# Kernel optimization log

Hardware: AMD Instinct MI355X
Metric: run time of the kernel (lower is better)

## Reference

```python
import jax, jax.numpy as jnp
import numpy as np
import math

D_MODEL = 128      # embedding_dim
D_STATE = 64
D_CONV = 4
NHEADS = 4         # d_inner / headdim (Mamba2 default headdim=64)
HEADDIM = 64
D_INNER = 256      # expand * d_model
CONV_DIM = 384     # d_inner + 2*ngroups*d_state (ngroups=1)
D_IN_PROJ = 644    # 2*d_inner + 2*ngroups*d_state + nheads
NLAYERS = 2
INPUT_DIM = 768
EPS = 1e-5


def setup_inputs() -> dict:
    key = jax.random.key(0)
    ks = jax.random.split(key, 20)
    rn = lambda k, s, sd=0.02: jax.random.normal(k, s, jnp.float32) * sd
    return {
        "x": jax.random.normal(ks[0], (16, 1024, INPUT_DIM), jnp.float32),
        "fc1_W": rn(ks[1], (INPUT_DIM, D_MODEL)),
        "fc1_b": jnp.zeros((D_MODEL,), jnp.float32),
        "ln_w": jnp.ones((NLAYERS, D_MODEL), jnp.float32),
        "ln_b": jnp.zeros((NLAYERS, D_MODEL), jnp.float32),
        "in_W": rn(ks[2], (NLAYERS, D_MODEL, D_IN_PROJ)),
        "conv_w": rn(ks[3], (NLAYERS, D_CONV, CONV_DIM), 0.1),
        "conv_b": jnp.zeros((NLAYERS, CONV_DIM), jnp.float32),
        "dt_bias": rn(ks[4], (NLAYERS, NHEADS), 0.5),
        "A_log": jnp.log(jax.random.uniform(ks[5], (NLAYERS, NHEADS), jnp.float32, 1.0, 16.0)),
        "Dp": jnp.ones((NLAYERS, NHEADS), jnp.float32),
        "rms_w": jnp.ones((NLAYERS, D_INNER), jnp.float32),
        "out_W": rn(ks[6], (NLAYERS, D_INNER, D_MODEL)),
        "fc2_W1": rn(ks[7], (D_MODEL, D_MODEL)),
        "fc2_b1": jnp.zeros((D_MODEL,), jnp.float32),
        "fc2_W2": rn(ks[8], (D_MODEL, 6)),
        "fc2_b2": jnp.zeros((6,), jnp.float32),
    }


def _pos_embedding(L):
    pos = jnp.arange(L, dtype=jnp.float32)[:, None]                       # (L,1)
    div = jnp.exp(jnp.arange(0, D_MODEL, 2, dtype=jnp.float32) * (-math.log(10000.0) / D_MODEL))
    pe = jnp.zeros((L, D_MODEL), jnp.float32)
    pe = pe.at[:, 0::2].set(jnp.sin(pos * div))
    pe = pe.at[:, 1::2].set(jnp.cos(pos * div))
    return pe[None]                                                        # (1,L,D)


def _layernorm(x, w, b):
    mu = jnp.mean(x, -1, keepdims=True)
    var = jnp.mean(jnp.square(x - mu), -1, keepdims=True)
    return (x - mu) * jax.lax.rsqrt(var + EPS) * w + b


def _mamba2(u, in_W, conv_w, conv_b, dt_bias, A_log, Dp, rms_w, out_W):
    b, l, _ = u.shape
    zxbcdt = u @ in_W                                                      # (b,l,644)
    z = zxbcdt[..., :D_INNER]
    xBC = zxbcdt[..., D_INNER:D_INNER + CONV_DIM]
    dt = jax.nn.softplus(zxbcdt[..., D_INNER + CONV_DIM:] + dt_bias)       # (b,l,h)
    # causal depthwise conv1d (width 4) + SiLU
    xp = jnp.pad(xBC, ((0, 0), (D_CONV - 1, 0), (0, 0)))
    xc = conv_b
    for k in range(D_CONV):
        xc = xc + conv_w[k] * xp[:, k:k + l, :]
    xc = jax.nn.silu(xc)                                                   # (b,l,384)
    xh = xc[..., :D_INNER].reshape(b, l, NHEADS, HEADDIM)                  # (b,l,h,p)
    B = xc[..., D_INNER:D_INNER + D_STATE]                                 # (b,l,n)
    C = xc[..., D_INNER + D_STATE:]                                        # (b,l,n)
    A = -jnp.exp(A_log)                                                    # (h,)
    dA = jnp.exp(dt * A)                                                   # (b,l,h)
    dtx = dt[..., None] * xh                                               # (b,l,h,p)

    def step(h, inp):
        dA_t, dtx_t, B_t, C_t = inp                                        # (b,h),(b,h,p),(b,n),(b,n)
        h = dA_t[..., None, None] * h + dtx_t[..., None] * B_t[:, None, None, :]
        y = jnp.einsum('bhpn,bn->bhp', h, C_t)
        return h, y

    h0 = jnp.zeros((b, NHEADS, HEADDIM, D_STATE), u.dtype)
    _, ys = jax.lax.scan(step, h0, (dA.transpose(1, 0, 2), dtx.transpose(1, 0, 2, 3),
                                    B.transpose(1, 0, 2), C.transpose(1, 0, 2)))
    y = ys.transpose(1, 0, 2, 3) + Dp[None, None, :, None] * xh            # (b,l,h,p)
    y = y.reshape(b, l, D_INNER)
    # gated RMSNorm: rmsnorm(y * silu(z)) * weight
    y = y * jax.nn.silu(z)
    y = y * jax.lax.rsqrt(jnp.mean(jnp.square(y), -1, keepdims=True) + EPS) * rms_w
    return y @ out_W


def reference(x, fc1_W, fc1_b, ln_w, ln_b, in_W, conv_w, conv_b, dt_bias,
              A_log, Dp, rms_w, out_W, fc2_W1, fc2_b1, fc2_W2, fc2_b2):
    h = x @ fc1_W + fc1_b                                                  # (b,l,128)
    h = h + _pos_embedding(h.shape[1])
    for i in range(NLAYERS):
        res = h
        hn = _layernorm(h, ln_w[i], ln_b[i])
        h = _mamba2(hn, in_W[i], conv_w[i], conv_b[i], dt_bias[i],
                    A_log[i], Dp[i], rms_w[i], out_W[i]) + res
        # dropout: identity in eval mode
    h = jax.nn.leaky_relu(h @ fc2_W1 + fc2_b1, negative_slope=0.1)
    return h @ fc2_W2 + fc2_b2                                             # (b,l,6)
```

## Files before the change

### kernel.cpp

```cpp
#include <hip/hip_runtime.h>
#include <hip/hip_bf16.h>

#define BATCH 16
#define SEQ 1024
#define NROWS (BATCH*SEQ)
#define IN_DIM 768
#define DM 128
#define DIP 644
#define DI 256
#define CDIM 384
#define DST 64
#define NH 4
#define HD 64
#define CHUNK 64
#define NCHUNK (SEQ/CHUNK)

#define WB_FC1   0
#define WB_IN    98304
#define WB_OUT   263168
#define WB_FC2   328704
#define WB_TOTAL 345088

typedef __attribute__((ext_vector_type(8))) short short8;
typedef __attribute__((ext_vector_type(4))) float float4v;

__device__ __forceinline__ short f2b(float f) {
    unsigned u = __builtin_bit_cast(unsigned, f);
    u += 0x7fffu + ((u >> 16) & 1u);
    return (short)(u >> 16);
}
__device__ __forceinline__ float s2f(short s) {
    unsigned u = ((unsigned)(unsigned short)s) << 16;
    return __builtin_bit_cast(float, u);
}
__device__ __forceinline__ short8 pack8f(float4 a, float4 b) {
    short8 r;
    r[0] = f2b(a.x); r[1] = f2b(a.y); r[2] = f2b(a.z); r[3] = f2b(a.w);
    r[4] = f2b(b.x); r[5] = f2b(b.y); r[6] = f2b(b.z); r[7] = f2b(b.w);
    return r;
}
__device__ __forceinline__ float silu(float a) { return a / (1.f + expf(-a)); }

__global__ void prep_weights(const float* __restrict__ fc1_W, const float* __restrict__ in_W,
                             const float* __restrict__ out_W, const float* __restrict__ fc2_W1,
                             short* __restrict__ wb) {
    int idx = blockIdx.x * 256 + threadIdx.x;
    if (idx < 98304) {
        int n = idx / 768, k = idx % 768;
        wb[WB_FC1 + idx] = f2b(fc1_W[k * 128 + n]);
        return;
    }
    idx -= 98304;
    if (idx < 2 * 82432) {
        int l = idx / 82432, r = idx % 82432;
        int n = r / 128, k = r % 128;
        wb[WB_IN + idx] = f2b(in_W[(size_t)l * 82432 + k * 644 + n]);
        return;
    }
    idx -= 164864;
    if (idx < 2 * 32768) {
        int l = idx / 32768, r = idx % 32768;
        int n = r / 256, k = r % 256;
        wb[WB_OUT + idx] = f2b(out_W[(size_t)l * 32768 + k * 128 + n]);
        return;
    }
    idx -= 65536;
    if (idx < 16384) {
        int n = idx / 128, k = idx % 128;
        wb[WB_FC2 + idx] = f2b(fc2_W1[k * 128 + n]);
    }
}

#define GEMM_PROLOGUE() \
    int tid = threadIdx.x; \
    int lane = tid & 63; \
    int m = lane & 15; \
    int kq = (lane >> 4) * 8; \
    int w = tid >> 6; \
    int mrow = (w & 3) * 16; \
    int ngrp = w >> 2; \
    int a_off = (mrow + m) * 72 + kq; \
    int b_off = (ngrp * 64 + m) * 72 + kq; \
    int ar = tid >> 3; \
    int ak = (tid & 7) * 8; \
    (void)ar; (void)ak; \
    float4v acc[4]; \
    acc[0] = (float4v)0.f; acc[1] = (float4v)0.f; acc[2] = (float4v)0.f; acc[3] = (float4v)0.f;

#define GEMM_COMPUTE_TILE() \
    { \
        short8 a0 = *reinterpret_cast<const short8*>(&As[a_off]); \
        short8 a1 = *reinterpret_cast<const short8*>(&As[a_off + 32]); \
        _Pragma("unroll") \
        for (int nt = 0; nt < 4; nt++) { \
            short8 b0 = *reinterpret_cast<const short8*>(&Bt[b_off + nt * 16 * 72]); \
            short8 b1 = *reinterpret_cast<const short8*>(&Bt[b_off + nt * 16 * 72 + 32]); \
            acc[nt] = __builtin_amdgcn_mfma_f32_16x16x32_bf16(a0, b0, acc[nt], 0, 0, 0); \
            acc[nt] = __builtin_amdgcn_mfma_f32_16x16x32_bf16(a1, b1, acc[nt], 0, 0, 0); \
        } \
    }

#define GEMM_STAGE_B(wtptr, LDB, k0) \
    _Pragma("unroll") \
    for (int i = 0; i < 2; i++) { \
        int idx = tid + i * 512; \
        int n = idx >> 3, kk = (idx & 7) * 8; \
        *reinterpret_cast<short8*>(&Bt[n * 72 + kk]) = \
            *reinterpret_cast<const short8*>(&wtptr[n * (LDB) + (k0) + kk]); \
    }

__global__ __launch_bounds__(512) void fc1_mfma(const float* __restrict__ x,
                                                const short* __restrict__ wt,
                                                const float* __restrict__ bias,
                                                const float* __restrict__ lnw0,
                                                const float* __restrict__ lnb0,
                                                float* __restrict__ h,
                                                short* __restrict__ hnb) {
    __shared__ __align__(16) char smem[64 * 133 * 4];
    short* As = (short*)smem;
    short* Bt = (short*)(smem + 64 * 72 * 2);
    float* hs = (float*)smem;
    GEMM_PROLOGUE();
    int row0 = blockIdx.x * 64;
    for (int kt = 0; kt < 12; kt++) {
        int k0 = kt * 64;
        if (kt) __syncthreads();
        {
            const float* src = x + (size_t)(row0 + ar) * IN_DIM + k0 + ak;
            float4 v0 = *(const float4*)src;
            float4 v1 = *(const float4*)(src + 4);
            *reinterpret_cast<short8*>(&As[ar * 72 + ak]) = pack8f(v0, v1);
        }
        GEMM_STAGE_B(wt, 768, k0);
        __syncthreads();
        GEMM_COMPUTE_TILE();
    }
    __syncthreads();
    #pragma unroll
    for (int nt = 0; nt < 4; nt++) {
        int col = ngrp * 64 + nt * 16 + m;
        float bv = bias[col];
        float div = expf(-(float)(col & ~1) * 0.071955784f);
        #pragma unroll
        for (int r = 0; r < 4; r++) {
            int rr = mrow + (lane >> 4) * 4 + r;
            int t = (row0 + rr) & (SEQ - 1);
            float arg = (float)t * div;
            float pe = (col & 1) ? cosf(arg) : sinf(arg);
            hs[rr * 133 + col] = acc[nt][r] + bv + pe;
        }
    }
    __syncthreads();
    {
        int r = tid >> 3, j = tid & 7;
        int row = row0 + r;
        float vals[16]; float s1 = 0.f, s2 = 0.f;
        #pragma unroll
        for (int i = 0; i < 16; i++) {
            float v = hs[r * 133 + j * 16 + i];
            vals[i] = v; s1 += v; s2 += v * v;
        }
        #pragma unroll
        for (int o = 1; o < 8; o <<= 1) { s1 += __shfl_xor(s1, o); s2 += __shfl_xor(s2, o); }
        float mu = s1 * (1.f / 128.f);
        float rs = rsqrtf(s2 * (1.f / 128.f) - mu * mu + 1e-5f);
        float* hdst = h + (size_t)row * DM + j * 16;
        #pragma unroll
        for (int i = 0; i < 4; i++)
            *(float4*)(hdst + i * 4) = make_float4(vals[i*4], vals[i*4+1], vals[i*4+2], vals[i*4+3]);
        const float* lw = lnw0 + j * 16;
        const float* lb = lnb0 + j * 16;
        short8 a0, a1;
        #pragma unroll
        for (int i = 0; i < 8; i++) {
            a0[i] = f2b((vals[i] - mu) * rs * lw[i] + lb[i]);
            a1[i] = f2b((vals[8 + i] - mu) * rs * lw[8 + i] + lb[8 + i]);
        }
        short* hndst = hnb + (size_t)row * DM + j * 16;
        *reinterpret_cast<short8*>(hndst) = a0;
        *reinterpret_cast<short8*>(hndst + 8) = a1;
    }
}

__global__ __launch_bounds__(512) void inproj_mfma(const short* __restrict__ hnb,
                                                   const short* __restrict__ wb,
                                                   short* __restrict__ zb,
                                                   short* __restrict__ xbc,
                                                   float* __restrict__ dtb,
                                                   const float* __restrict__ dt_bias, int layer) {
    __shared__ short As[64 * 72];
    __shared__ short Bt[128 * 72];
    GEMM_PROLOGUE();
    int row0 = blockIdx.x * 64;
    int ncol0 = blockIdx.y * 128;
    const short* wt = wb + WB_IN + (size_t)layer * 82432;
    for (int kt = 0; kt < 2; kt++) {
        int k0 = kt * 64;
        if (kt) __syncthreads();
        *reinterpret_cast<short8*>(&As[ar * 72 + ak]) =
            *reinterpret_cast<const short8*>(&hnb[(size_t)(row0 + ar) * DM + k0 + ak]);
        #pragma unroll
        for (int i = 0; i < 2; i++) {
            int idx = tid + i * 512;
            int n = idx >> 3, kk = (idx & 7) * 8;
            int col = ncol0 + n;
            short8 bv = (short8)0;
            if (col < DIP) bv = *reinterpret_cast<const short8*>(&wt[col * 128 + k0 + kk]);
            *reinterpret_cast<short8*>(&Bt[n * 72 + kk]) = bv;
        }
        __syncthreads();
        GEMM_COMPUTE_TILE();
    }
    #pragma unroll
    for (int nt = 0; nt < 4; nt++) {
        int col = ncol0 + ngrp * 64 + nt * 16 + m;
        if (col < DI) {
            #pragma unroll
            for (int r = 0; r < 4; r++) {
                int row = row0 + mrow + (lane >> 4) * 4 + r;
                zb[(size_t)row * DI + col] = f2b(acc[nt][r]);
            }
        } else if (col < DI + CDIM) {
            #pragma unroll
            for (int r = 0; r < 4; r++) {
                int row = row0 + mrow + (lane >> 4) * 4 + r;
                xbc[(size_t)row * CDIM + (col - DI)] = f2b(acc[nt][r]);
            }
        } else if (col < DIP) {
            int hh = col - DI - CDIM;
            float db = dt_bias[layer * NH + hh];
            #pragma unroll
            for (int r = 0; r < 4; r++) {
                int row = row0 + mrow + (lane >> 4) * 4 + r;
                float raw = acc[nt][r] + db;
                float dt = (raw > 20.f) ? raw : log1pf(expf(raw));
                dtb[(size_t)row * NH + hh] = dt;
            }
        }
    }
}

__global__ void conv_kernel(const short* __restrict__ xbc,
                            const float* __restrict__ convw, const float* __restrict__ convb,
                            short* __restrict__ xcb, int layer) {
    int c = threadIdx.x;
    int row0 = blockIdx.x * 4;
    int l0 = row0 & (SEQ - 1);
    const float* cw = convw + (size_t)layer * 4 * CDIM;
    float w0 = cw[c], w1 = cw[CDIM + c], w2 = cw[2 * CDIM + c], w3 = cw[3 * CDIM + c];
    float bb = convb[layer * CDIM + c];
    float v[7];
    #pragma unroll
    for (int i = 0; i < 7; i++) {
        int rr = row0 + i - 3;
        v[i] = (l0 + i - 3 >= 0) ? s2f(xbc[(size_t)rr * CDIM + c]) : 0.f;
    }
    #pragma unroll
    for (int j = 0; j < 4; j++) {
        float acc = bb + w0 * v[j] + w1 * v[j + 1] + w2 * v[j + 2] + w3 * v[j + 3];
        xcb[(size_t)(row0 + j) * CDIM + c] = f2b(silu(acc));
    }
}

__global__ __launch_bounds__(256) void chunk_state_mfma(const short* __restrict__ xcb,
                                                        const float* __restrict__ dtb,
                                                        const float* __restrict__ A_log,
                                                        short* __restrict__ Slocb,
                                                        float* __restrict__ decay, int layer) {
    __shared__ short XTw[64 * 72];
    __shared__ short BT[64 * 72];
    __shared__ float wst[64];
    int bid = blockIdx.x;
    int c  = bid & (NCHUNK - 1);
    int hh = (bid >> 4) & (NH - 1);
    int b  = bid >> 6;
    int tid = threadIdx.x;
    int row0 = b * SEQ + c * CHUNK;
    float A = -expf(A_log[layer * NH + hh]);

    if (tid < CHUNK) {
        float dtv = dtb[(size_t)(row0 + tid) * NH + hh];
        float l = dtv * A;
        #pragma unroll
        for (int o = 1; o < 64; o <<= 1) { float v = __shfl_up(l, o); if (tid >= o) l += v; }
        float Ltot = __shfl(l, 63);
        wst[tid] = expf(Ltot - l) * dtv;
        if (tid == 63) decay[bid] = expf(Ltot);
    }
    __syncthreads();
    {
        int p = tid & 63;
        int tb0 = tid >> 6;
        #pragma unroll
        for (int i = 0; i < 2; i++) {
            int t0 = (tb0 + i * 4) * 8;
            short8 xv, bv;
            #pragma unroll
            for (int j = 0; j < 8; j++) {
                int t = t0 + j;
                const short* xr = xcb + (size_t)(row0 + t) * CDIM;
                xv[j] = f2b(s2f(xr[hh * HD + p]) * wst[t]);
                bv[j] = xr[DI + p];
            }
            *reinterpret_cast<short8*>(&XTw[p * 72 + t0]) = xv;
            *reinterpret_cast<short8*>(&BT[p * 72 + t0]) = bv;
        }
    }
    __syncthreads();

    int lane = tid & 63;
    int m = lane & 15;
    int kq = (lane >> 4) * 8;
    int w = tid >> 6;
    int a_off = (w * 16 + m) * 72 + kq;
    float4v acc[4];
    acc[0] = (float4v)0.f; acc[1] = (float4v)0.f; acc[2] = (float4v)0.f; acc[3] = (float4v)0.f;
    short8 a0 = *reinterpret_cast<const short8*>(&XTw[a_off]);
    short8 a1 = *reinterpret_cast<const short8*>(&XTw[a_off + 32]);
    #pragma unroll
    for (int nt = 0; nt < 4; nt++) {
        int bo = (nt * 16 + m) * 72 + kq;
        short8 b0 = *reinterpret_cast<const short8*>(&BT[bo]);
        short8 b1 = *reinterpret_cast<const short8*>(&BT[bo + 32]);
        acc[nt] = __builtin_amdgcn_mfma_f32_16x16x32_bf16(a0, b0, acc[nt], 0, 0, 0);
        acc[nt] = __builtin_amdgcn_mfma_f32_16x16x32_bf16(a1, b1, acc[nt], 0, 0, 0);
    }
    short* Sp = Slocb + (size_t)bid * (HD * DST);
    int tq = (lane >> 4) * 4;
    #pragma unroll
    for (int nt = 0; nt < 4; nt++) {
        #pragma unroll
        for (int r = 0; r < 4; r++) {
            int p = w * 16 + tq + r;
            int n = nt * 16 + m;
            Sp[p * DST + n] = f2b(acc[nt][r]);
        }
    }
}

__global__ void chunk_scan_kernel(const short* __restrict__ Slocb, const float* __restrict__ decay,
                                  short* __restrict__ hstrb) {
    int bh = blockIdx.x;
    int tid = threadIdx.x;
    float hreg[16];
    #pragma unroll
    for (int k = 0; k < 16; k++) hreg[k] = 0.f;
    for (int c = 0; c < NCHUNK; c++) {
        size_t base = ((size_t)bh * NCHUNK + c) * (HD * DST) + tid * 16;
        float d = decay[bh * NCHUNK + c];
        short8 s0 = *reinterpret_cast<const short8*>(&Slocb[base]);
        short8 s1 = *reinterpret_cast<const short8*>(&Slocb[base + 8]);
        short8 h0, h1;
        #pragma unroll
        for (int k = 0; k < 8; k++) { h0[k] = f2b(hreg[k]); h1[k] = f2b(hreg[8 + k]); }
        *reinterpret_cast<short8*>(&hstrb[base]) = h0;
        *reinterpret_cast<short8*>(&hstrb[base + 8]) = h1;
        #pragma unroll
        for (int k = 0; k < 8; k++) {
            hreg[k]     = d * hreg[k]     + s2f(s0[k]);
            hreg[8 + k] = d * hreg[8 + k] + s2f(s1[k]);
        }
    }
}

__global__ __launch_bounds__(256) void chunk_out_mfma(const short* __restrict__ xcb,
                                                      const float* __restrict__ dtb,
                                                      const float* __restrict__ A_log,
                                                      const float* __restrict__ Dpw,
                                                      const short* __restrict__ hstrb,
                                                      short* __restrict__ ybb, int layer) {
    __shared__ short Cb[64 * 72];
    __shared__ short Bb[64 * 72];
    __shared__ short XT[64 * 72];
    __shared__ short HT[64 * 72];
    __shared__ float Ls[64], dts[64];
    int bid = blockIdx.x;
    int c  = bid & (NCHUNK - 1);
    int hh = (bid >> 4) & (NH - 1);
    int b  = bid >> 6;
    int tid = threadIdx.x;
    int row0 = b * SEQ + c * CHUNK;
    float A = -expf(A_log[layer * NH + hh]);
    float Dph = Dpw[layer * NH + hh];

    if (tid < CHUNK) {
        float dtv = dtb[(size_t)(row0 + tid) * NH + hh];
        float l = dtv * A;
        #pragma unroll
        for (int o = 1; o < 64; o <<= 1) { float v = __shfl_up(l, o); if (tid >= o) l += v; }
        Ls[tid] = l;
        dts[tid] = dtv;
    }
    {
        int p = tid & 63;
        int tb0 = tid >> 6;
        #pragma unroll
        for (int i = 0; i < 2; i++) {
            int t0 = (tb0 + i * 4) * 8;
            short8 xv;
            #pragma unroll
            for (int j = 0; j < 8; j++)
                xv[j] = xcb[(size_t)(row0 + t0 + j) * CDIM + hh * HD + p];
            *reinterpret_cast<short8*>(&XT[p * 72 + t0]) = xv;
        }
    }
    #pragma unroll
    for (int i = 0; i < 2; i++) {
        int idx = tid + i * 256;
        int t = idx >> 3, cb = (idx & 7) * 8;
        const short* xr = xcb + (size_t)(row0 + t) * CDIM;
        *reinterpret_cast<short8*>(&Bb[t * 72 + cb]) =
            *reinterpret_cast<const short8*>(&xr[DI + cb]);
        *reinterpret_cast<short8*>(&Cb[t * 72 + cb]) =
            *reinterpret_cast<const short8*>(&xr[DI + DST + cb]);
    }
    {
        const short* hs = hstrb + (size_t)bid * (HD * DST);
        #pragma unroll
        for (int i = 0; i < 2; i++) {
            int idx = tid + i * 256;
            int pp = idx >> 3, nb = (idx & 7) * 8;
            *reinterpret_cast<short8*>(&HT[pp * 72 + nb]) =
                *reinterpret_cast<const short8*>(&hs[pp * 64 + nb]);
        }
    }
    __syncthreads();

    int lane = tid & 63;
    int m = lane & 15;
    int kq = (lane >> 4) * 8;
    int w = tid >> 6;
    int tq = (lane >> 4) * 4;
    int a_off = (w * 16 + m) * 72 + kq;

    short8 ca0 = *reinterpret_cast<const short8*>(&Cb[a_off]);
    short8 ca1 = *reinterpret_cast<const short8*>(&Cb[a_off + 32]);

    float4v g[4], ir[4];
    #pragma unroll
    for (int i = 0; i < 4; i++) { g[i] = (float4v)0.f; ir[i] = (float4v)0.f; }
    #pragma unroll
    for (int st = 0; st < 4; st++) {
        int bo = (st * 16 + m) * 72 + kq;
        short8 b0 = *reinterpret_cast<const short8*>(&Bb[bo]);
        short8 b1 = *reinterpret_cast<const short8*>(&Bb[bo + 32]);
        g[st] = __builtin_amdgcn_mfma_f32_16x16x32_bf16(ca0, b0, g[st], 0, 0, 0);
        g[st] = __builtin_amdgcn_mfma_f32_16x16x32_bf16(ca1, b1, g[st], 0, 0, 0);
        short8 h0 = *reinterpret_cast<const short8*>(&HT[bo]);
        short8 h1 = *reinterpret_cast<const short8*>(&HT[bo + 32]);
        ir[st] = __builtin_amdgcn_mfma_f32_16x16x32_bf16(ca0, h0, ir[st], 0, 0, 0);
        ir[st] = __builtin_amdgcn_mfma_f32_16x16x32_bf16(ca1, h1, ir[st], 0, 0, 0);
    }
    __syncthreads();
    #pragma unroll
    for (int st = 0; st < 4; st++) {
        #pragma unroll
        for (int r = 0; r < 4; r++) {
            int t = w * 16 + tq + r;
            int s = st * 16 + m;
            float mv = 0.f;
            if (s <= t) mv = g[st][r] * expf(Ls[t] - Ls[s]) * dts[s];
            Bb[t * 72 + s] = f2b(mv);
        }
    }
    __syncthreads();
    float4v yi[4];
    #pragma unroll
    for (int i = 0; i < 4; i++) yi[i] = (float4v)0.f;
    short8 ma0 = *reinterpret_cast<const short8*>(&Bb[a_off]);
    short8 ma1 = *reinterpret_cast<const short8*>(&Bb[a_off + 32]);
    #pragma unroll
    for (int pt = 0; pt < 4; pt++) {
        int bo = (pt * 16 + m) * 72 + kq;
        short8 x0 = *reinterpret_cast<const short8*>(&XT[bo]);
        short8 x1 = *reinterpret_cast<const short8*>(&XT[bo + 32]);
        yi[pt] = __builtin_amdgcn_mfma_f32_16x16x32_bf16(ma0, x0, yi[pt], 0, 0, 0);
        yi[pt] = __builtin_amdgcn_mfma_f32_16x16x32_bf16(ma1, x1, yi[pt], 0, 0, 0);
    }
    #pragma unroll
    for (int r = 0; r < 4; r++) {
        int t = w * 16 + tq + r;
        float et = expf(Ls[t]);
        short* yr = ybb + (size_t)(row0 + t) * DI + hh * HD;
        #pragma unroll
        for (int pt = 0; pt < 4; pt++) {
            int p = pt * 16 + m;
            float xv = s2f(XT[p * 72 + t]);
            yr[p] = f2b(yi[pt][r] + et * ir[pt][r] + Dph * xv);
        }
    }
}

__global__ __launch_bounds__(512) void outproj_gate_mfma(const short* __restrict__ ybb,
                                                         const short* __restrict__ zb,
                                                         const float* __restrict__ rmsw,
                                                         const short* __restrict__ wb,
                                                         const float* __restrict__ lnw2,
                                                         const float* __restrict__ lnb2,
                                                         float* __restrict__ h,
                                                         short* __restrict__ hnb,
                                                         int layer, int write_hn) {
    __shared__ __align__(16) char smem[64 * 133 * 4];
    short* As = (short*)smem;
    short* Bt = (short*)(smem + 64 * 72 * 2);
    float* hs = (float*)smem;
    __shared__ float rs_s[64];
    GEMM_PROLOGUE();
    int row0 = blockIdx.x * 64;
    const short* wt = wb + WB_OUT + (size_t)layer * 32768;
    {
        int r = tid >> 3, j = tid & 7;
        const short8* yr = (const short8*)(ybb + (size_t)(row0 + r) * DI + j * 32);
        const short8* zr = (const short8*)(zb + (size_t)(row0 + r) * DI + j * 32);
        float s2 = 0.f;
        #pragma unroll
        for (int i = 0; i < 4; i++) {
            short8 yv = yr[i];
            short8 zv = zr[i];
            #pragma unroll
            for (int q = 0; q < 8; q++) {
                float v = s2f(yv[q]) * silu(s2f(zv[q]));
                s2 += v * v;
            }
        }
        #pragma unroll
        for (int o = 1; o < 8; o <<= 1) s2 += __shfl_xor(s2, o);
        if (j == 0) rs_s[r] = rsqrtf(s2 * (1.f / 256.f) + 1e-5f);
    }
    __syncthreads();
    for (int kt = 0; kt < 4; kt++) {
        int k0 = kt * 64;
        if (kt) __syncthreads();
        {
            int k = k0 + ak;
            short8 yv = *(const short8*)(ybb + (size_t)(row0 + ar) * DI + k);
            short8 zv = *(const short8*)(zb + (size_t)(row0 + ar) * DI + k);
            float4 w0 = *(const float4*)(rmsw + layer * DI + k);
            float4 w1 = *(const float4*)(rmsw + layer * DI + k + 4);
            float rs = rs_s[ar];
            short8 av;
            av[0] = f2b(s2f(yv[0]) * silu(s2f(zv[0])) * rs * w0.x);
            av[1] = f2b(s2f(yv[1]) * silu(s2f(zv[1])) * rs * w0.y);
            av[2] = f2b(s2f(yv[2]) * silu(s2f(zv[2])) * rs * w0.z);
            av[3] = f2b(s2f(yv[3]) * silu(s2f(zv[3])) * rs * w0.w);
            av[4] = f2b(s2f(yv[4]) * silu(s2f(zv[4])) * rs * w1.x);
            av[5] = f2b(s2f(yv[5]) * silu(s2f(zv[5])) * rs * w1.y);
            av[6] = f2b(s2f(yv[6]) * silu(s2f(zv[6])) * rs * w1.z);
            av[7] = f2b(s2f(yv[7]) * silu(s2f(zv[7])) * rs * w1.w);
            *reinterpret_cast<short8*>(&As[ar * 72 + ak]) = av;
        }
        GEMM_STAGE_B(wt, 256, k0);
        __syncthreads();
        GEMM_COMPUTE_TILE();
    }
    __syncthreads();
    #pragma unroll
    for (int nt = 0; nt < 4; nt++) {
        int col = ngrp * 64 + nt * 16 + m;
        #pragma unroll
        for (int r = 0; r < 4; r++) {
            int rr = mrow + (lane >> 4) * 4 + r;
            hs[rr * 133 + col] = acc[nt][r];
        }
    }
    __syncthreads();
    {
        int r = tid >> 3, j = tid & 7;
        int row = row0 + r;
        float* hdst = h + (size_t)row * DM + j * 16;
        float vals[16]; float s1 = 0.f, s2 = 0.f;
        #pragma unroll
        for (int i = 0; i < 4; i++) {
            float4 ho = *(const float4*)(hdst + i * 4);
            float v0 = ho.x + hs[r * 133 + j * 16 + i * 4];
            float v1 = ho.y + hs[r * 133 + j * 16 + i * 4 + 1];
            float v2 = ho.z + hs[r * 133 + j * 16 + i * 4 + 2];
            float v3 = ho.w + hs[r * 133 + j * 16 + i * 4 + 3];
            vals[i*4] = v0; vals[i*4+1] = v1; vals[i*4+2] = v2; vals[i*4+3] = v3;
            s1 += v0 + v1 + v2 + v3;
            s2 += v0*v0 + v1*v1 + v2*v2 + v3*v3;
        }
        #pragma unroll
        for (int o = 1; o < 8; o <<= 1) { s1 += __shfl_xor(s1, o); s2 += __shfl_xor(s2, o); }
        #pragma unroll
        for (int i = 0; i < 4; i++)
            *(float4*)(hdst + i * 4) = make_float4(vals[i*4], vals[i*4+1], vals[i*4+2], vals[i*4+3]);
        if (write_hn) {
            float mu = s1 * (1.f / 128.f);
            float rs = rsqrtf(s2 * (1.f / 128.f) - mu * mu + 1e-5f);
            const float* lw = lnw2 + j * 16;
            const float* lb = lnb2 + j * 16;
            short8 a0, a1;
            #pragma unroll
            for (int i = 0; i < 8; i++) {
                a0[i] = f2b((vals[i] - mu) * rs * lw[i] + lb[i]);
                a1[i] = f2b((vals[8 + i] - mu) * rs * lw[8 + i] + lb[8 + i]);
            }
            short* hndst = hnb + (size_t)row * DM + j * 16;
            *reinterpret_cast<short8*>(hndst) = a0;
            *reinterpret_cast<short8*>(hndst + 8) = a1;
        }
    }
}

__global__ __launch_bounds__(512) void fc2ab_mfma(const float* __restrict__ h,
                                                  const short* __restrict__ wb,
                                                  const float* __restrict__ b1,
                                                  const float* __restrict__ W2,
                                                  const float* __restrict__ b2,
                                                  float* __restrict__ out) {
    __shared__ short As[64 * 72];
    __shared__ short Bt[128 * 72];
    __shared__ float h2s[64][132];
    __shared__ float w2s[768];
    GEMM_PROLOGUE();
    int row0 = blockIdx.x * 64;
    const short* wt = wb + WB_FC2;
    for (int i = tid; i < 768; i += 512) w2s[i] = W2[i];
    for (int kt = 0; kt < 2; kt++) {
        int k0 = kt * 64;
        if (kt) __syncthreads();
        {
            const float* src = h + (size_t)(row0 + ar) * DM + k0 + ak;
            float4 v0 = *(const float4*)src;
            float4 v1 = *(const float4*)(src + 4);
            *reinterpret_cast<short8*>(&As[ar * 72 + ak]) = pack8f(v0, v1);
        }
        GEMM_STAGE_B(wt, 128, k0);
        __syncthreads();
        GEMM_COMPUTE_TILE();
    }
    #pragma unroll
    for (int nt = 0; nt < 4; nt++) {
        int col = ngrp * 64 + nt * 16 + m;
        float bv = b1[col];
        #pragma unroll
        for (int r = 0; r < 4; r++) {
            int rr = mrow + (lane >> 4) * 4 + r;
            float o = acc[nt][r] + bv;
            h2s[rr][col] = (o > 0.f) ? o : 0.1f * o;
        }
    }
    __syncthreads();
    if (tid < 384) {
        int r = tid / 6, cc = tid % 6;
        float acc2 = b2[cc];
        #pragma unroll 16
        for (int k = 0; k < 128; k++) acc2 += h2s[r][k] * w2s[k * 6 + cc];
        out[(size_t)(row0 + r) * 6 + cc] = acc2;
    }
}

extern "C" void kernel_launch(void* const* d_in, const int* in_sizes, int n_in,
                              void* d_out, int out_size, void* d_ws, size_t ws_size,
                              hipStream_t stream) {
    const float* x       = (const float*)d_in[0];
    const float* fc1_W   = (const float*)d_in[1];
    const float* fc1_b   = (const float*)d_in[2];
    const float* ln_w    = (const float*)d_in[3];
    const float* ln_b    = (const float*)d_in[4];
    const float* in_W    = (const float*)d_in[5];
    const float* conv_w  = (const float*)d_in[6];
    const float* conv_b  = (const float*)d_in[7];
    const float* dt_bias = (const float*)d_in[8];
    const float* A_log   = (const float*)d_in[9];
    const float* Dp      = (const float*)d_in[10];
    const float* rms_w   = (const float*)d_in[11];
    const float* out_W   = (const float*)d_in[12];
    const float* fc2_W1  = (const float*)d_in[13];
    const float* fc2_b1  = (const float*)d_in[14];
    const float* fc2_W2  = (const float*)d_in[15];
    const float* fc2_b2  = (const float*)d_in[16];
    float* out = (float*)d_out;

    float* ws = (float*)d_ws;
    float* h     = ws;
    float* dtb   = h     + (size_t)NROWS * DM;
    float* decay = dtb   + (size_t)NROWS * NH;
    short* sbase = (short*)(decay + 1024);
    short* hnb   = sbase;
    short* zb    = hnb   + (size_t)NROWS * DM;
    short* xbc   = zb    + (size_t)NROWS * DI;
    short* xcb   = xbc   + (size_t)NROWS * CDIM;
    short* ybb   = xcb   + (size_t)NROWS * CDIM;
    short* Slocb = ybb   + (size_t)NROWS * DI;
    short* hstrb = Slocb + (size_t)BATCH*NH*NCHUNK*HD*DST;
    short* wb    = hstrb + (size_t)BATCH*NH*NCHUNK*HD*DST;

    prep_weights<<<1348, 256, 0, stream>>>(fc1_W, in_W, out_W, fc2_W1, wb);
    fc1_mfma<<<NROWS / 64, 512, 0, stream>>>(x, wb + WB_FC1, fc1_b, ln_w, ln_b, h, hnb);

    for (int layer = 0; layer < 2; layer++) {
        inproj_mfma<<<dim3(NROWS / 64, 6), 512, 0, stream>>>(hnb, wb, zb, xbc, dtb,
                                                             dt_bias, layer);
        conv_kernel<<<NROWS / 4, CDIM, 0, stream>>>(xbc, conv_w, conv_b, xcb, layer);
        chunk_state_mfma<<<BATCH*NH*NCHUNK, 256, 0, stream>>>(xcb, dtb, A_log, Slocb, decay, layer);
        chunk_scan_kernel<<<BATCH*NH, 256, 0, stream>>>(Slocb, decay, hstrb);
        chunk_out_mfma<<<BATCH*NH*NCHUNK, 256, 0, stream>>>(xcb, dtb, A_log, Dp, hstrb, ybb, layer);
        outproj_gate_mfma<<<NROWS / 64, 512, 0, stream>>>(ybb, zb, rms_w, wb,
                                                          ln_w + DM, ln_b + DM, h, hnb,
                                                          layer, layer == 0 ? 1 : 0);
    }

    fc2ab_mfma<<<NROWS / 64, 512, 0, stream>>>(h, wb, fc2_b1, fc2_W2, fc2_b2, out);
}
```

Before: 269.1 us.

## Shrink row tiles to 32 and do LayerNorm epilogue in registers

```diff
diff --git a/kernel.cpp b/kernel.cpp
--- a/kernel.cpp
+++ b/kernel.cpp
@@ -100,28 +100,29 @@
         } \
     }
 
-#define GEMM_STAGE_B(wtptr, LDB, k0) \
-    _Pragma("unroll") \
-    for (int i = 0; i < 2; i++) { \
-        int idx = tid + i * 512; \
-        int n = idx >> 3, kk = (idx & 7) * 8; \
-        *reinterpret_cast<short8*>(&Bt[n * 72 + kk]) = \
-            *reinterpret_cast<const short8*>(&wtptr[n * (LDB) + (k0) + kk]); \
-    }
-
-__global__ __launch_bounds__(512) void fc1_mfma(const float* __restrict__ x,
+__global__ __launch_bounds__(256) void fc1_mfma(const float* __restrict__ x,
                                                 const short* __restrict__ wt,
                                                 const float* __restrict__ bias,
                                                 const float* __restrict__ lnw0,
                                                 const float* __restrict__ lnb0,
                                                 float* __restrict__ h,
                                                 short* __restrict__ hnb) {
-    __shared__ __align__(16) char smem[64 * 133 * 4];
-    short* As = (short*)smem;
-    short* Bt = (short*)(smem + 64 * 72 * 2);
-    float* hs = (float*)smem;
-    GEMM_PROLOGUE();
-    int row0 = blockIdx.x * 64;
+    __shared__ short As[32 * 72];
+    __shared__ short Bt[128 * 72];
+    __shared__ float ps1[32][2], ps2[32][2];
+    int tid = threadIdx.x;
+    int lane = tid & 63;
+    int m = lane & 15;
+    int quad = lane >> 4;
+    int kq = quad * 8;
+    int w = tid >> 6;
+    int mrow = (w & 1) * 16;
+    int ngrp = w >> 1;
+    int ar = tid >> 3;
+    int ak = (tid & 7) * 8;
+    int row0 = blockIdx.x * 32;
+    float4v acc[4];
+    acc[0] = (float4v)0.f; acc[1] = (float4v)0.f; acc[2] = (float4v)0.f; acc[3] = (float4v)0.f;
     for (int kt = 0; kt < 12; kt++) {
         int k0 = kt * 64;
         if (kt) __syncthreads();
@@ -131,11 +132,27 @@
             float4 v1 = *(const float4*)(src + 4);
             *reinterpret_cast<short8*>(&As[ar * 72 + ak]) = pack8f(v0, v1);
         }
-        GEMM_STAGE_B(wt, 768, k0);
+        #pragma unroll
+        for (int i = 0; i < 4; i++) {
+            int idx = tid + i * 256;
+            int n = idx >> 3, kk = (idx & 7) * 8;
+            *reinterpret_cast<short8*>(&Bt[n * 72 + kk]) =
+                *reinterpret_cast<const short8*>(&wt[n * 768 + k0 + kk]);
+        }
         __syncthreads();
-        GEMM_COMPUTE_TILE();
-    }
-    __syncthreads();
+        short8 a0 = *reinterpret_cast<const short8*>(&As[(mrow + m) * 72 + kq]);
+        short8 a1 = *reinterpret_cast<const short8*>(&As[(mrow + m) * 72 + kq + 32]);
+        #pragma unroll
+        for (int nt = 0; nt < 4; nt++) {
+            int bo = (ngrp * 64 + nt * 16 + m) * 72 + kq;
+            short8 b0 = *reinterpret_cast<const short8*>(&Bt[bo]);
+            short8 b1 = *reinterpret_cast<const short8*>(&Bt[bo + 32]);
+            acc[nt] = __builtin_amdgcn_mfma_f32_16x16x32_bf16(a0, b0, acc[nt], 0, 0, 0);
+            acc[nt] = __builtin_amdgcn_mfma_f32_16x16x32_bf16(a1, b1, acc[nt], 0, 0, 0);
+        }
+    }
+    float val[4][4];
+    float s1r[4] = {0.f,0.f,0.f,0.f}, s2r[4] = {0.f,0.f,0.f,0.f};
     #pragma unroll
     for (int nt = 0; nt < 4; nt++) {
         int col = ngrp * 64 + nt * 16 + m;
@@ -143,42 +160,46 @@
         float div = expf(-(float)(col & ~1) * 0.071955784f);
         #pragma unroll
         for (int r = 0; r < 4; r++) {
-            int rr = mrow + (lane >> 4) * 4 + r;
-            int t = (row0 + rr) & (SEQ - 1);
+            int row = row0 + mrow + quad * 4 + r;
+            int t = row & (SEQ - 1);
             float arg = (float)t * div;
             float pe = (col & 1) ? cosf(arg) : sinf(arg);
-            hs[rr * 133 + col] = acc[nt][r] + bv + pe;
-        }
-    }
-    __syncthreads();
-    {
-        int r = tid >> 3, j = tid & 7;
-        int row = row0 + r;
-        float vals[16]; float s1 = 0.f, s2 = 0.f;
-        #pragma unroll
-        for (int i = 0; i < 16; i++) {
-            float v = hs[r * 133 + j * 16 + i];
-            vals[i] = v; s1 += v; s2 += v * v;
-        }
-        #pragma unroll
-        for (int o = 1; o < 8; o <<= 1) { s1 += __shfl_xor(s1, o); s2 += __shfl_xor(s2, o); }
+            float v = acc[nt][r] + bv + pe;
+            val[nt][r] = v;
+            s1r[r] += v; s2r[r] += v * v;
+        }
+    }
+    #pragma unroll
+    for (int o = 1; o < 16; o <<= 1) {
+        #pragma unroll
+        for (int r = 0; r < 4; r++) {
+            s1r[r] += __shfl_xor(s1r[r], o);
+            s2r[r] += __shfl_xor(s2r[r], o);
+        }
+    }
+    if (m == 0) {
+        #pragma unroll
+        for (int r = 0; r < 4; r++) {
+            ps1[mrow + quad * 4 + r][ngrp] = s1r[r];
+            ps2[mrow + quad * 4 + r][ngrp] = s2r[r];
+        }
+    }
+    __syncthreads();
+    #pragma unroll
+    for (int r = 0; r < 4; r++) {
+        int rl = mrow + quad * 4 + r;
+        float s1 = ps1[rl][0] + ps1[rl][1];
+        float s2 = ps2[rl][0] + ps2[rl][1];
         float mu = s1 * (1.f / 128.f);
         float rs = rsqrtf(s2 * (1.f / 128.f) - mu * mu + 1e-5f);
-        float* hdst = h + (size_t)row * DM + j * 16;
-        #pragma unroll
-        for (int i = 0; i < 4; i++)
-            *(float4*)(hdst + i * 4) = make_float4(vals[i*4], vals[i*4+1], vals[i*4+2], vals[i*4+3]);
-        const float* lw = lnw0 + j * 16;
-        const float* lb = lnb0 + j * 16;
-        short8 a0, a1;
-        #pragma unroll
-        for (int i = 0; i < 8; i++) {
-            a0[i] = f2b((vals[i] - mu) * rs * lw[i] + lb[i]);
-            a1[i] = f2b((vals[8 + i] - mu) * rs * lw[8 + i] + lb[8 + i]);
-        }
-        short* hndst = hnb + (size_t)row * DM + j * 16;
-        *reinterpret_cast<short8*>(hndst) = a0;
-        *reinterpret_cast<short8*>(hndst + 8) = a1;
+        int row = row0 + rl;
+        #pragma unroll
+        for (int nt = 0; nt < 4; nt++) {
+            int col = ngrp * 64 + nt * 16 + m;
+            float v = val[nt][r];
+            h[(size_t)row * DM + col] = v;
+            hnb[(size_t)row * DM + col] = f2b((v - mu) * rs * lnw0[col] + lnb0[col]);
+        }
     }
 }
 
@@ -491,7 +512,7 @@
     }
 }
 
-__global__ __launch_bounds__(512) void outproj_gate_mfma(const short* __restrict__ ybb,
+__global__ __launch_bounds__(256) void outproj_gate_mfma(const short* __restrict__ ybb,
                                                          const short* __restrict__ zb,
                                                          const float* __restrict__ rmsw,
                                                          const short* __restrict__ wb,
@@ -500,13 +521,21 @@
                                                          float* __restrict__ h,
                                                          short* __restrict__ hnb,
                                                          int layer, int write_hn) {
-    __shared__ __align__(16) char smem[64 * 133 * 4];
-    short* As = (short*)smem;
-    short* Bt = (short*)(smem + 64 * 72 * 2);
-    float* hs = (float*)smem;
-    __shared__ float rs_s[64];
-    GEMM_PROLOGUE();
-    int row0 = blockIdx.x * 64;
+    __shared__ short As[32 * 72];
+    __shared__ short Bt[128 * 72];
+    __shared__ float rs_s[32];
+    __shared__ float ps1[32][2], ps2[32][2];
+    int tid = threadIdx.x;
+    int lane = tid & 63;
+    int m = lane & 15;
+    int quad = lane >> 4;
+    int kq = quad * 8;
+    int w = tid >> 6;
+    int mrow = (w & 1) * 16;
+    int ngrp = w >> 1;
+    int ar = tid >> 3;
+    int ak = (tid & 7) * 8;
+    int row0 = blockIdx.x * 32;
     const short* wt = wb + WB_OUT + (size_t)layer * 32768;
     {
         int r = tid >> 3, j = tid & 7;
@@ -528,6 +557,8 @@
         if (j == 0) rs_s[r] = rsqrtf(s2 * (1.f / 256.f) + 1e-5f);
     }
     __syncthreads();
+    float4v acc[4];
+    acc[0] = (float4v)0.f; acc[1] = (float4v)0.f; acc[2] = (float4v)0.f; acc[3] = (float4v)0.f;
     for (int kt = 0; kt < 4; kt++) {
         int k0 = kt * 64;
         if (kt) __syncthreads();
@@ -549,74 +580,98 @@
             av[7] = f2b(s2f(yv[7]) * silu(s2f(zv[7])) * rs * w1.w);
             *reinterpret_cast<short8*>(&As[ar * 72 + ak]) = av;
         }
-        GEMM_STAGE_B(wt, 256, k0);
+        #pragma unroll
+        for (int i = 0; i < 4; i++) {
+            int idx = tid + i * 256;
+            int n = idx >> 3, kk = (idx & 7) * 8;
+            *reinterpret_cast<short8*>(&Bt[n * 72 + kk]) =
+                *reinterpret_cast<const short8*>(&wt[n * 256 + k0 + kk]);
+        }
         __syncthreads();
-        GEMM_COMPUTE_TILE();
-    }
-    __syncthreads();
+        short8 a0 = *reinterpret_cast<const short8*>(&As[(mrow + m) * 72 + kq]);
+        short8 a1 = *reinterpret_cast<const short8*>(&As[(mrow + m) * 72 + kq + 32]);
+        #pragma unroll
+        for (int nt = 0; nt < 4; nt++) {
+            int bo = (ngrp * 64 + nt * 16 + m) * 72 + kq;
+            short8 b0 = *reinterpret_cast<const short8*>(&Bt[bo]);
+            short8 b1 = *reinterpret_cast<const short8*>(&Bt[bo + 32]);
+            acc[nt] = __builtin_amdgcn_mfma_f32_16x16x32_bf16(a0, b0, acc[nt], 0, 0, 0);
+            acc[nt] = __builtin_amdgcn_mfma_f32_16x16x32_bf16(a1, b1, acc[nt], 0, 0, 0);
+        }
+    }
+    float val[4][4];
+    float s1r[4] = {0.f,0.f,0.f,0.f}, s2r[4] = {0.f,0.f,0.f,0.f};
     #pragma unroll
     for (int nt = 0; nt < 4; nt++) {
         int col = ngrp * 64 + nt * 16 + m;
         #pragma unroll
         for (int r = 0; r < 4; r++) {
-            int rr = mrow + (lane >> 4) * 4 + r;
-            hs[rr * 133 + col] = acc[nt][r];
-        }
-    }
-    __syncthreads();
-    {
-        int r = tid >> 3, j = tid & 7;
-        int row = row0 + r;
-        float* hdst = h + (size_t)row * DM + j * 16;
-        float vals[16]; float s1 = 0.f, s2 = 0.f;
-        #pragma unroll
-        for (int i = 0; i < 4; i++) {
-            float4 ho = *(const float4*)(hdst + i * 4);
-            float v0 = ho.x + hs[r * 133 + j * 16 + i * 4];
-            float v1 = ho.y + hs[r * 133 + j * 16 + i * 4 + 1];
-            float v2 = ho.z + hs[r * 133 + j * 16 + i * 4 + 2];
-            float v3 = ho.w + hs[r * 133 + j * 16 + i * 4 + 3];
-            vals[i*4] = v0; vals[i*4+1] = v1; vals[i*4+2] = v2; vals[i*4+3] = v3;
-            s1 += v0 + v1 + v2 + v3;
-            s2 += v0*v0 + v1*v1 + v2*v2 + v3*v3;
-        }
-        #pragma unroll
-        for (int o = 1; o < 8; o <<= 1) { s1 += __shfl_xor(s1, o); s2 += __shfl_xor(s2, o); }
-        #pragma unroll
-        for (int i = 0; i < 4; i++)
-            *(float4*)(hdst + i * 4) = make_float4(vals[i*4], vals[i*4+1], vals[i*4+2], vals[i*4+3]);
-        if (write_hn) {
-            float mu = s1 * (1.f / 128.f);
-            float rs = rsqrtf(s2 * (1.f / 128.f) - mu * mu + 1e-5f);
-            const float* lw = lnw2 + j * 16;
-            const float* lb = lnb2 + j * 16;
-            short8 a0, a1;
-            #pragma unroll
-            for (int i = 0; i < 8; i++) {
-                a0[i] = f2b((vals[i] - mu) * rs * lw[i] + lb[i]);
-                a1[i] = f2b((vals[8 + i] - mu) * rs * lw[8 + i] + lb[8 + i]);
-            }
-            short* hndst = hnb + (size_t)row * DM + j * 16;
-            *reinterpret_cast<short8*>(hndst) = a0;
-            *reinterpret_cast<short8*>(hndst + 8) = a1;
-        }
-    }
-}
-
-__global__ __launch_bounds__(512) void fc2ab_mfma(const float* __restrict__ h,
+            int row = row0 + mrow + quad * 4 + r;
+            float v = h[(size_t)row * DM + col] + acc[nt][r];
+            val[nt][r] = v;
+            s1r[r] += v; s2r[r] += v * v;
+        }
+    }
+    #pragma unroll
+    for (int o = 1; o < 16; o <<= 1) {
+        #pragma unroll
+        for (int r = 0; r < 4; r++) {
+            s1r[r] += __shfl_xor(s1r[r], o);
+            s2r[r] += __shfl_xor(s2r[r], o);
+        }
+    }
+    if (m == 0) {
+        #pragma unroll
+        for (int r = 0; r < 4; r++) {
+            ps1[mrow + quad * 4 + r][ngrp] = s1r[r];
+            ps2[mrow + quad * 4 + r][ngrp] = s2r[r];
+        }
+    }
+    __syncthreads();
+    #pragma unroll
+    for (int r = 0; r < 4; r++) {
+        int rl = mrow + quad * 4 + r;
+        int row = row0 + rl;
+        float s1 = ps1[rl][0] + ps1[rl][1];
+        float s2 = ps2[rl][0] + ps2[rl][1];
+        float mu = s1 * (1.f / 128.f);
+        float rs = rsqrtf(s2 * (1.f / 128.f) - mu * mu + 1e-5f);
+        #pragma unroll
+        for (int nt = 0; nt < 4; nt++) {
+            int col = ngrp * 64 + nt * 16 + m;
+            float v = val[nt][r];
+            h[(size_t)row * DM + col] = v;
+            if (write_hn)
+                hnb[(size_t)row * DM + col] = f2b((v - mu) * rs * lnw2[col] + lnb2[col]);
+        }
+    }
+}
+
+__global__ __launch_bounds__(256) void fc2ab_mfma(const float* __restrict__ h,
                                                   const short* __restrict__ wb,
                                                   const float* __restrict__ b1,
                                                   const float* __restrict__ W2,
                                                   const float* __restrict__ b2,
                                                   float* __restrict__ out) {
-    __shared__ short As[64 * 72];
+    __shared__ short As[32 * 72];
     __shared__ short Bt[128 * 72];
-    __shared__ float h2s[64][132];
+    __shared__ float h2s[32][132];
     __shared__ float w2s[768];
-    GEMM_PROLOGUE();
-    int row0 = blockIdx.x * 64;
+    int tid = threadIdx.x;
+    int lane = tid & 63;
+    int m = lane & 15;
+    int quad = lane >> 4;
+    int kq = quad * 8;
+    int w = tid >> 6;
+    int mrow = (w & 1) * 16;
+    int ngrp = w >> 1;
+    int ar = tid >> 3;
+    int ak = (tid & 7) * 8;
+    int row0 = blockIdx.x * 32;
     const short* wt = wb + WB_FC2;
-    for (int i = tid; i < 768; i += 512) w2s[i] = W2[i];
+    for (int i = tid; i < 768; i += 256) w2s[i] = W2[i];
+    float4v acc[4];
+    acc[0] = (float4v)0.f; acc[1] = (float4v)0.f; acc[2] = (float4v)0.f; acc[3] = (float4v)0.f;
     for (int kt = 0; kt < 2; kt++) {
         int k0 = kt * 64;
         if (kt) __syncthreads();
@@ -626,23 +681,39 @@
             float4 v1 = *(const float4*)(src + 4);
             *reinterpret_cast<short8*>(&As[ar * 72 + ak]) = pack8f(v0, v1);
         }
-        GEMM_STAGE_B(wt, 128, k0);
+        #pragma unroll
+        for (int i = 0; i < 4; i++) {
+            int idx = tid + i * 256;
+            int n = idx >> 3, kk = (idx & 7) * 8;
+            *reinterpret_cast<short8*>(&Bt[n * 72 + kk]) =
+                *reinterpret_cast<const short8*>(&wt[n * 128 + k0 + kk]);
+        }
         __syncthreads();
-        GEMM_COMPUTE_TILE();
-    }
+        short8 a0 = *reinterpret_cast<const short8*>(&As[(mrow + m) * 72 + kq]);
+        short8 a1 = *reinterpret_cast<const short8*>(&As[(mrow + m) * 72 + kq + 32]);
+        #pragma unroll
+        for (int nt = 0; nt < 4; nt++) {
+            int bo = (ngrp * 64 + nt * 16 + m) * 72 + kq;
+            short8 b0 = *reinterpret_cast<const short8*>(&Bt[bo]);
+            short8 b1 = *reinterpret_cast<const short8*>(&Bt[bo + 32]);
+            acc[nt] = __builtin_amdgcn_mfma_f32_16x16x32_bf16(a0, b0, acc[nt], 0, 0, 0);
+            acc[nt] = __builtin_amdgcn_mfma_f32_16x16x32_bf16(a1, b1, acc[nt], 0, 0, 0);
+        }
+    }
+    __syncthreads();
     #pragma unroll
     for (int nt = 0; nt < 4; nt++) {
         int col = ngrp * 64 + nt * 16 + m;
         float bv = b1[col];
         #pragma unroll
         for (int r = 0; r < 4; r++) {
-            int rr = mrow + (lane >> 4) * 4 + r;
+            int rr = mrow + quad * 4 + r;
             float o = acc[nt][r] + bv;
             h2s[rr][col] = (o > 0.f) ? o : 0.1f * o;
         }
     }
     __syncthreads();
-    if (tid < 384) {
+    if (tid < 192) {
         int r = tid / 6, cc = tid % 6;
         float acc2 = b2[cc];
         #pragma unroll 16
@@ -688,7 +759,7 @@
     short* wb    = hstrb + (size_t)BATCH*NH*NCHUNK*HD*DST;
 
     prep_weights<<<1348, 256, 0, stream>>>(fc1_W, in_W, out_W, fc2_W1, wb);
-    fc1_mfma<<<NROWS / 64, 512, 0, stream>>>(x, wb + WB_FC1, fc1_b, ln_w, ln_b, h, hnb);
+    fc1_mfma<<<NROWS / 32, 256, 0, stream>>>(x, wb + WB_FC1, fc1_b, ln_w, ln_b, h, hnb);
 
     for (int layer = 0; layer < 2; layer++) {
         inproj_mfma<<<dim3(NROWS / 64, 6), 512, 0, stream>>>(hnb, wb, zb, xbc, dtb,
@@ -697,10 +768,10 @@
         chunk_state_mfma<<<BATCH*NH*NCHUNK, 256, 0, stream>>>(xcb, dtb, A_log, Slocb, decay, layer);
         chunk_scan_kernel<<<BATCH*NH, 256, 0, stream>>>(Slocb, decay, hstrb);
         chunk_out_mfma<<<BATCH*NH*NCHUNK, 256, 0, stream>>>(xcb, dtb, A_log, Dp, hstrb, ybb, layer);
-        outproj_gate_mfma<<<NROWS / 64, 512, 0, stream>>>(ybb, zb, rms_w, wb,
+        outproj_gate_mfma<<<NROWS / 32, 256, 0, stream>>>(ybb, zb, rms_w, wb,
                                                           ln_w + DM, ln_b + DM, h, hnb,
                                                           layer, layer == 0 ? 1 : 0);
     }
 
-    fc2ab_mfma<<<NROWS / 64, 512, 0, stream>>>(h, wb, fc2_b1, fc2_W2, fc2_b2, out);
-}
+    fc2ab_mfma<<<NROWS / 32, 256, 0, stream>>>(h, wb, fc2_b1, fc2_W2, fc2_b2, out);
+}
```

After: 275.7 us. +2.4%, slower.

## Shrink fc1 row tile to 32 and fuse LayerNorm via register reductions

Applied to the files above, without the earlier changes.

```diff
diff --git a/kernel.cpp b/kernel.cpp
--- a/kernel.cpp
+++ b/kernel.cpp
@@ -116,69 +116,94 @@
                                                 const float* __restrict__ lnb0,
                                                 float* __restrict__ h,
                                                 short* __restrict__ hnb) {
-    __shared__ __align__(16) char smem[64 * 133 * 4];
-    short* As = (short*)smem;
-    short* Bt = (short*)(smem + 64 * 72 * 2);
-    float* hs = (float*)smem;
-    GEMM_PROLOGUE();
-    int row0 = blockIdx.x * 64;
+    __shared__ short As[32 * 72];
+    __shared__ short Bt[128 * 72];
+    __shared__ float ps1[32][4], ps2[32][4];
+    int tid = threadIdx.x;
+    int lane = tid & 63;
+    int m = lane & 15;
+    int quad = lane >> 4;
+    int kq = quad * 8;
+    int w = tid >> 6;
+    int mrow = (w & 1) * 16;
+    int ngrp = w >> 1;
+    int ar = tid >> 4;
+    int ac = (tid & 15) * 4;
+    int row0 = blockIdx.x * 32;
+    float4v acc[2];
+    acc[0] = (float4v)0.f; acc[1] = (float4v)0.f;
     for (int kt = 0; kt < 12; kt++) {
         int k0 = kt * 64;
         if (kt) __syncthreads();
         {
-            const float* src = x + (size_t)(row0 + ar) * IN_DIM + k0 + ak;
-            float4 v0 = *(const float4*)src;
-            float4 v1 = *(const float4*)(src + 4);
-            *reinterpret_cast<short8*>(&As[ar * 72 + ak]) = pack8f(v0, v1);
+            const float* src = x + (size_t)(row0 + ar) * IN_DIM + k0 + ac;
+            float4 v = *(const float4*)src;
+            short4 pv;
+            pv.x = f2b(v.x); pv.y = f2b(v.y); pv.z = f2b(v.z); pv.w = f2b(v.w);
+            *reinterpret_cast<short4*>(&As[ar * 72 + ac]) = pv;
         }
         GEMM_STAGE_B(wt, 768, k0);
         __syncthreads();
-        GEMM_COMPUTE_TILE();
-    }
-    __syncthreads();
-    #pragma unroll
-    for (int nt = 0; nt < 4; nt++) {
-        int col = ngrp * 64 + nt * 16 + m;
+        short8 a0 = *reinterpret_cast<const short8*>(&As[(mrow + m) * 72 + kq]);
+        short8 a1 = *reinterpret_cast<const short8*>(&As[(mrow + m) * 72 + kq + 32]);
+        #pragma unroll
+        for (int nt = 0; nt < 2; nt++) {
+            int bo = (ngrp * 32 + nt * 16 + m) * 72 + kq;
+            short8 b0 = *reinterpret_cast<const short8*>(&Bt[bo]);
+            short8 b1 = *reinterpret_cast<const short8*>(&Bt[bo + 32]);
+            acc[nt] = __builtin_amdgcn_mfma_f32_16x16x32_bf16(a0, b0, acc[nt], 0, 0, 0);
+            acc[nt] = __builtin_amdgcn_mfma_f32_16x16x32_bf16(a1, b1, acc[nt], 0, 0, 0);
+        }
+    }
+    float val[2][4];
+    float s1r[4] = {0.f,0.f,0.f,0.f}, s2r[4] = {0.f,0.f,0.f,0.f};
+    #pragma unroll
+    for (int nt = 0; nt < 2; nt++) {
+        int col = ngrp * 32 + nt * 16 + m;
         float bv = bias[col];
         float div = expf(-(float)(col & ~1) * 0.071955784f);
         #pragma unroll
         for (int r = 0; r < 4; r++) {
-            int rr = mrow + (lane >> 4) * 4 + r;
-            int t = (row0 + rr) & (SEQ - 1);
+            int row = row0 + mrow + quad * 4 + r;
+            int t = row & (SEQ - 1);
             float arg = (float)t * div;
             float pe = (col & 1) ? cosf(arg) : sinf(arg);
-            hs[rr * 133 + col] = acc[nt][r] + bv + pe;
-        }
-    }
-    __syncthreads();
-    {
-        int r = tid >> 3, j = tid & 7;
-        int row = row0 + r;
-        float vals[16]; float s1 = 0.f, s2 = 0.f;
-        #pragma unroll
-        for (int i = 0; i < 16; i++) {
-            float v = hs[r * 133 + j * 16 + i];
-            vals[i] = v; s1 += v; s2 += v * v;
-        }
-        #pragma unroll
-        for (int o = 1; o < 8; o <<= 1) { s1 += __shfl_xor(s1, o); s2 += __shfl_xor(s2, o); }
+            float v = acc[nt][r] + bv + pe;
+            val[nt][r] = v;
+            s1r[r] += v; s2r[r] += v * v;
+        }
+    }
+    #pragma unroll
+    for (int o = 1; o < 16; o <<= 1) {
+        #pragma unroll
+        for (int r = 0; r < 4; r++) {
+            s1r[r] += __shfl_xor(s1r[r], o);
+            s2r[r] += __shfl_xor(s2r[r], o);
+        }
+    }
+    if (m == 0) {
+        #pragma unroll
+        for (int r = 0; r < 4; r++) {
+            ps1[mrow + quad * 4 + r][ngrp] = s1r[r];
+            ps2[mrow + quad * 4 + r][ngrp] = s2r[r];
+        }
+    }
+    __syncthreads();
+    #pragma unroll
+    for (int r = 0; r < 4; r++) {
+        int rl = mrow + quad * 4 + r;
+        float s1 = ps1[rl][0] + ps1[rl][1] + ps1[rl][2] + ps1[rl][3];
+        float s2 = ps2[rl][0] + ps2[rl][1] + ps2[rl][2] + ps2[rl][3];
         float mu = s1 * (1.f / 128.f);
         float rs = rsqrtf(s2 * (1.f / 128.f) - mu * mu + 1e-5f);
-        float* hdst = h + (size_t)row * DM + j * 16;
-        #pragma unroll
-        for (int i = 0; i < 4; i++)
-            *(float4*)(hdst + i * 4) = make_float4(vals[i*4], vals[i*4+1], vals[i*4+2], vals[i*4+3]);
-        const float* lw = lnw0 + j * 16;
-        const float* lb = lnb0 + j * 16;
-        short8 a0, a1;
-        #pragma unroll
-        for (int i = 0; i < 8; i++) {
-            a0[i] = f2b((vals[i] - mu) * rs * lw[i] + lb[i]);
-            a1[i] = f2b((vals[8 + i] - mu) * rs * lw[8 + i] + lb[8 + i]);
-        }
-        short* hndst = hnb + (size_t)row * DM + j * 16;
-        *reinterpret_cast<short8*>(hndst) = a0;
-        *reinterpret_cast<short8*>(hndst + 8) = a1;
+        int row = row0 + rl;
+        #pragma unroll
+        for (int nt = 0; nt < 2; nt++) {
+            int col = ngrp * 32 + nt * 16 + m;
+            float v = val[nt][r];
+            h[(size_t)row * DM + col] = v;
+            hnb[(size_t)row * DM + col] = f2b((v - mu) * rs * lnw0[col] + lnb0[col]);
+        }
     }
 }
 
@@ -688,7 +713,7 @@
     short* wb    = hstrb + (size_t)BATCH*NH*NCHUNK*HD*DST;
 
     prep_weights<<<1348, 256, 0, stream>>>(fc1_W, in_W, out_W, fc2_W1, wb);
-    fc1_mfma<<<NROWS / 64, 512, 0, stream>>>(x, wb + WB_FC1, fc1_b, ln_w, ln_b, h, hnb);
+    fc1_mfma<<<NROWS / 32, 512, 0, stream>>>(x, wb + WB_FC1, fc1_b, ln_w, ln_b, h, hnb);
 
     for (int layer = 0; layer < 2; layer++) {
         inproj_mfma<<<dim3(NROWS / 64, 6), 512, 0, stream>>>(hnb, wb, zb, xbc, dtb,
```

Result: faster. 261.4 us (-2.9%).
